# Kernel optimization log

Measured on AMD Instinct MI355X. Metric: run time of the kernel, lower is better.

## Reference

```python
import jax, jax.numpy as jnp
import numpy as np

N = 50000      # nodes
E = 800000     # edges
H = 128        # hidden_channels
L = 3          # num_layers
G = 128        # graphs in batch
MAXZ = 1000    # max_z


def layer_norm(x, g, b, eps=1e-5):
    m = x.mean(-1, keepdims=True)
    v = ((x - m) ** 2).mean(-1, keepdims=True)
    return (x - m) / jnp.sqrt(v + eps) * g + b


def setup_inputs() -> dict:
    key = jax.random.key(0)
    ks = jax.random.split(key, 16)
    z = jax.random.randint(ks[0], (N,), 0, 3)
    edge_index = jax.random.randint(ks[1], (2, E), 0, N)
    batch = jnp.sort(jax.random.randint(ks[2], (N,), 0, G))
    sc = 1.0 / np.sqrt(H)
    z_table = jax.random.normal(ks[3], (MAXZ, H), jnp.float32) * 0.05
    W1s = jax.random.normal(ks[4], (L, H, H), jnp.float32) * sc
    b1s = jnp.zeros((L, H), jnp.float32)
    W2s = jax.random.normal(ks[5], (L, H, H), jnp.float32) * sc
    b2s = jnp.zeros((L, H), jnp.float32)
    lng = jnp.ones((L, H), jnp.float32)
    lnb = jnp.zeros((L, H), jnp.float32)
    lin0_W = jax.random.normal(ks[6], (L * H, H), jnp.float32) * (1.0 / np.sqrt(L * H))
    lin0_b = jnp.zeros((H,), jnp.float32)
    linA_W = jax.random.normal(ks[7], (H, H), jnp.float32) * sc
    linA_b = jnp.zeros((H,), jnp.float32)
    linB_W = jax.random.normal(ks[8], (H, 1), jnp.float32) * sc
    linB_b = jnp.zeros((1,), jnp.float32)
    return dict(z=z, edge_index=edge_index, batch=batch, z_table=z_table,
                W1s=W1s, b1s=b1s, W2s=W2s, b2s=b2s, lng=lng, lnb=lnb,
                lin0_W=lin0_W, lin0_b=lin0_b, linA_W=linA_W, linA_b=linA_b,
                linB_W=linB_W, linB_b=linB_b)


def reference(z, edge_index, batch, z_table, W1s, b1s, W2s, b2s, lng, lnb,
              lin0_W, lin0_b, linA_W, linA_b, linB_W, linB_b):
    # z_emb indices: ([[1],[2]] == z) -> {0,1}, shape [2, N]
    idx = jnp.stack([(z == 1), (z == 2)]).astype(jnp.int32)
    x = z_table[idx]                                  # [2, N, H]
    src, dst = edge_index[0], edge_index[1]
    xs = []
    for l in range(L):
        # GINConv, eps=0: MLP(x + scatter_add of neighbor features)
        agg = jnp.zeros_like(x).at[:, dst].add(x[:, src])   # [2, N, H]
        h = x + agg
        h = jax.nn.relu(h @ W1s[l] + b1s[l])
        h = jax.nn.relu(h @ W2s[l] + b2s[l])
        x = layer_norm(h, lng[l], lnb[l])
        xs.append(x)
    x = jnp.concatenate(xs, axis=-1)                  # [2, N, L*H] (JK)
    # lin0 (dropout = identity in eval), then sum over the label dim
    x = jax.nn.relu(x @ lin0_W + lin0_b).sum(axis=0)  # [N, H]
    # global mean pool over graphs
    sums = jax.ops.segment_sum(x, batch, num_segments=G)                       # [G, H]
    cnt = jax.ops.segment_sum(jnp.ones((x.shape[0], 1), x.dtype), batch, num_segments=G)
    x = sums / jnp.maximum(cnt, 1.0)
    x = jax.nn.relu(x @ linA_W + linA_b)
    return x @ linB_W + linB_b                        # [G, 1]
```

## Files before the change

### kernel.cpp

```cpp
#include <hip/hip_runtime.h>
#include <math.h>

#define NN 50000
#define EE 800000
#define HH 128
#define LL 3
#define GG 128
#define MM (2*NN)
#define PB1 1024

typedef unsigned int u32;
typedef unsigned short u16;
using s16x8 = __attribute__((ext_vector_type(8))) short;
using f32x4 = __attribute__((ext_vector_type(4))) float;

__device__ __forceinline__ u16 f2bf(float f){
  u32 u = __float_as_uint(f);
  return (u16)((u + 0x7fffu + ((u >> 16) & 1u)) >> 16);
}
__device__ __forceinline__ float bf2f(u16 h){ return __uint_as_float(((u32)h) << 16); }
__device__ __forceinline__ u32 splitpack(float v){
  u16 h = f2bf(v);
  float r = v - bf2f(h);
  u16 l = f2bf(r);
  return (u32)h | ((u32)l << 16);
}
__device__ __forceinline__ float unpack2(u32 u){
  return __uint_as_float(u << 16) + __uint_as_float(u & 0xffff0000u);
}

__global__ void zero_i32(int* p, int n){
  int i = blockIdx.x*blockDim.x + threadIdx.x;
  if (i < n) p[i] = 0;
}

__global__ void deg_kernel(const int* __restrict__ ei, int* __restrict__ deg){
  int e = blockIdx.x*blockDim.x + threadIdx.x;
  if (e < EE) atomicAdd(&deg[ei[EE + e]], 1);
}

__global__ void scan_kernel(const int* deg, int* rowstart, int* cursor, int n){
  __shared__ int wsum[16], woff[16];
  __shared__ int carry_s;
  const int tid = threadIdx.x, lane = tid & 63, wid = tid >> 6;
  if (tid == 0) carry_s = 0;
  __syncthreads();
  for (int base = 0; base < n; base += 4096){
    int i4 = base + tid*4;
    int4 v = make_int4(0,0,0,0);
    if (i4 + 3 < n) v = *(const int4*)&deg[i4];
    else {
      if (i4+0 < n) v.x = deg[i4+0];
      if (i4+1 < n) v.y = deg[i4+1];
      if (i4+2 < n) v.z = deg[i4+2];
      if (i4+3 < n) v.w = deg[i4+3];
    }
    int s = v.x + v.y + v.z + v.w;
    int incl = s;
    #pragma unroll
    for (int off = 1; off < 64; off <<= 1){
      int t = __shfl_up(incl, off);
      if (lane >= off) incl += t;
    }
    if (lane == 63) wsum[wid] = incl;
    __syncthreads();
    if (tid < 16){
      int wv = wsum[tid];
      int winc = wv;
      #pragma unroll
      for (int off = 1; off < 16; off <<= 1){
        int t = __shfl_up(winc, off);
        if (tid >= off) winc += t;
      }
      woff[tid] = winc - wv;
    }
    __syncthreads();
    int c = carry_s;
    int excl = c + woff[wid] + incl - s;
    if (i4 < n){
      int p = excl;
      rowstart[i4] = p; cursor[i4] = p; p += v.x;
      if (i4+1 < n){ rowstart[i4+1] = p; cursor[i4+1] = p; p += v.y; }
      if (i4+2 < n){ rowstart[i4+2] = p; cursor[i4+2] = p; p += v.z; }
      if (i4+3 < n){ rowstart[i4+3] = p; cursor[i4+3] = p; }
    }
    __syncthreads();
    if (tid == 1023) carry_s = c + woff[15] + incl;
    __syncthreads();
  }
  if (tid == 0) rowstart[n] = carry_s;
}

__global__ void scatter_kernel(const int* __restrict__ ei, int* __restrict__ cursor,
                               int* __restrict__ csr){
  int e = blockIdx.x*blockDim.x + threadIdx.x;
  if (e < EE){
    int d = ei[EE + e];
    int w = atomicAdd(&cursor[d], 1);
    csr[w] = ei[e];
  }
}

__global__ void prep_w(const float* __restrict__ W1s, const float* __restrict__ W2s,
                       const float* __restrict__ lin0W, u16* __restrict__ wt){
  int idx = blockIdx.x*256 + threadIdx.x;
  int srcsel = idx / 49152;
  int r = idx - srcsel*49152;
  int k = r >> 7, c = r & 127;
  const float* src = srcsel==0 ? W1s : (srcsel==1 ? W2s : lin0W);
  float v = src[r];
  u16 h = f2bf(v);
  u16 l = f2bf(v - bf2f(h));
  if (srcsel < 2){
    int ly = k >> 7, kk = k & 127;
    size_t o = (size_t)srcsel*98304 + (size_t)ly*32768 + (size_t)c*128 + kk;
    wt[o] = h; wt[o + 16384] = l;
  } else {
    size_t o = 196608 + (size_t)c*384 + k;
    wt[o] = h; wt[o + 49152] = l;
  }
}

template<bool L0>
__global__ void agg_kernel(const int* __restrict__ rowstart, const int* __restrict__ csr,
                           const int* __restrict__ z, const float* __restrict__ ztab,
                           const u16* __restrict__ xin,
                           u32* __restrict__ hout){
  const int lane = threadIdx.x & 63;
  const int n    = blockIdx.x*4 + (threadIdx.x >> 6);
  const int e0 = rowstart[n], e1 = rowstart[n+1];
  if (L0){
    const int f2 = lane*2;
    float2 t0 = *(const float2*)&ztab[f2];
    float2 t1 = *(const float2*)&ztab[HH + f2];
    int c1 = 0, c2 = 0;
    for (int base = e0; base < e1; base += 64){
      if (base + lane < e1){
        int zs = z[csr[base + lane]];
        c1 += (zs == 1); c2 += (zs == 2);
      }
    }
    #pragma unroll
    for (int off = 1; off < 64; off <<= 1){
      c1 += __shfl_xor(c1, off);
      c2 += __shfl_xor(c2, off);
    }
    int zn  = z[n];
    int deg = e1 - e0;
    float w1a = (float)((zn == 1) + c1), w0a = (float)((zn != 1) + deg - c1);
    float w1b = (float)((zn == 2) + c2), w0b = (float)((zn != 2) + deg - c2);
    float2 acc0, acc1;
    acc0.x = w1a*t1.x + w0a*t0.x;  acc0.y = w1a*t1.y + w0a*t0.y;
    acc1.x = w1b*t1.x + w0b*t0.x;  acc1.y = w1b*t1.y + w0b*t0.y;
    *(uint2*)(hout + (size_t)n*HH + f2) =
        make_uint2(splitpack(acc0.x), splitpack(acc0.y));
    *(uint2*)(hout + (size_t)(NN + n)*HH + f2) =
        make_uint2(splitpack(acc1.x), splitpack(acc1.y));
  } else {
    const u16* base = xin + lane*4;
    ushort4 sv = *(const ushort4*)(base + (size_t)n*256);
    float4 acc;
    acc.x = bf2f(sv.x); acc.y = bf2f(sv.y);
    acc.z = bf2f(sv.z); acc.w = bf2f(sv.w);
    for (int b = e0; b < e1; b += 64){
      int m  = (e1 - b < 64) ? (e1 - b) : 64;
      int sl = (b + lane < e1) ? csr[b + lane] : 0;
      #pragma unroll 4
      for (int j = 0; j < m; ++j){
        int s = __shfl(sl, j);
        ushort4 v = *(const ushort4*)(base + (size_t)s*256);
        acc.x += bf2f(v.x); acc.y += bf2f(v.y);
        acc.z += bf2f(v.z); acc.w += bf2f(v.w);
      }
    }
    uint4 o;
    o.x = splitpack(acc.x); o.y = splitpack(acc.y);
    o.z = splitpack(acc.z); o.w = splitpack(acc.w);
    const int ch = lane >> 5, f = (lane & 31)*4;
    *(uint4*)(hout + ((size_t)ch*NN + n)*HH + f) = o;
  }
}

template<int K, int MODE>
__global__ __launch_bounds__(256, 4)
void gemm_mfma(const void* __restrict__ Asp,
               const u16* __restrict__ WtHi, const u16* __restrict__ WtLo,
               const float* __restrict__ bias,
               const float* __restrict__ gamma, const float* __restrict__ beta,
               u16* __restrict__ C16, float* __restrict__ Cf){
  constexpr bool ASPLIT = (MODE == 0);
  __shared__ u16 lds[16384];
  const int tid  = threadIdx.x;
  const int lane = tid & 63, w = tid >> 6;
  const int r16  = lane & 15, g = lane >> 4;
  const int rowBase = blockIdx.x * 128;

  f32x4 acc[2][8];
  #pragma unroll
  for (int i = 0; i < 2; i++)
    #pragma unroll
    for (int j = 0; j < 8; j++) acc[i][j] = (f32x4){0.f,0.f,0.f,0.f};

  const int sr = tid & 127;
  const int kq = tid >> 7;
  const int arow = rowBase + sr;
  const bool avalid = arow < MM;
  const int ach = arow >= NN ? 1 : 0;
  const int an  = arow - ach*NN;

  const u16* whi = WtHi + (size_t)sr*K + kq*16;
  const u16* wlo = WtLo + (size_t)sr*K + kq*16;

  for (int kc = 0; kc < K; kc += 32){
    const int k0 = kc + kq*16;
    if (ASPLIT){
      const u32* ap = (const u32*)Asp + (size_t)arow*128 + k0;
      #pragma unroll
      for (int q = 0; q < 4; q++){
        uint4 av = make_uint4(0,0,0,0);
        if (avalid) av = *(const uint4*)(ap + q*4);
        u32 h01 = (av.x & 0xffffu) | (av.y << 16);
        u32 h23 = (av.z & 0xffffu) | (av.w << 16);
        u32 l01 = (av.x >> 16) | (av.y & 0xffff0000u);
        u32 l23 = (av.z >> 16) | (av.w & 0xffff0000u);
        int k = kq*16 + q*4;
        int base = ((k >> 3)*128 + sr)*8 + (k & 7);
        *(uint2*)&lds[base]        = make_uint2(h01, h23);
        *(uint2*)&lds[4096 + base] = make_uint2(l01, l23);
      }
    } else {
      const u16* ap;
      if (MODE == 2)
        ap = (const u16*)Asp + ((size_t)(k0 >> 7))*NN*256 + (size_t)an*256 + ach*128 + (k0 & 127);
      else
        ap = (const u16*)Asp + (size_t)arow*128 + k0;
      #pragma unroll
      for (int hg = 0; hg < 2; hg++){
        uint4 av = make_uint4(0,0,0,0);
        if (avalid) av = *(const uint4*)(ap + hg*8);
        *(uint4*)&lds[((kq*2 + hg)*128 + sr)*8] = av;
      }
    }
    #pragma unroll
    for (int hg = 0; hg < 2; hg++){
      int gsel = kq*2 + hg;
      *(uint4*)&lds[8192  + (gsel*128 + sr)*8] = *(const uint4*)(whi + kc + hg*8);
      *(uint4*)&lds[12288 + (gsel*128 + sr)*8] = *(const uint4*)(wlo + kc + hg*8);
    }
    __syncthreads();
    s16x8 ahi[2], alo[2];
    #pragma unroll
    for (int i = 0; i < 2; i++){
      int idx = (g*128 + w*32 + i*16 + r16)*8;
      ahi[i] = *(const s16x8*)&lds[idx];
      if (ASPLIT) alo[i] = *(const s16x8*)&lds[4096 + idx];
    }
    #pragma unroll
    for (int j = 0; j < 8; j++){
      int bidx = (g*128 + j*16 + r16)*8;
      s16x8 bhi = *(const s16x8*)&lds[8192  + bidx];
      s16x8 blo = *(const s16x8*)&lds[12288 + bidx];
      #pragma unroll
      for (int i = 0; i < 2; i++){
        acc[i][j] = __builtin_amdgcn_mfma_f32_16x16x32_bf16(ahi[i], bhi, acc[i][j], 0, 0, 0);
        acc[i][j] = __builtin_amdgcn_mfma_f32_16x16x32_bf16(ahi[i], blo, acc[i][j], 0, 0, 0);
        if (ASPLIT)
          acc[i][j] = __builtin_amdgcn_mfma_f32_16x16x32_bf16(alo[i], bhi, acc[i][j], 0, 0, 0);
      }
    }
    __syncthreads();
  }

  float bb[8];
  #pragma unroll
  for (int j = 0; j < 8; j++) bb[j] = bias[j*16 + r16];
  #pragma unroll
  for (int i = 0; i < 2; i++)
    #pragma unroll
    for (int j = 0; j < 8; j++)
      #pragma unroll
      for (int c = 0; c < 4; c++){
        float t = acc[i][j][c] + bb[j];
        acc[i][j][c] = t > 0.f ? t : 0.f;
      }

  if (MODE == 1){
    float gg_[8], be[8];
    #pragma unroll
    for (int j = 0; j < 8; j++){ gg_[j] = gamma[j*16 + r16]; be[j] = beta[j*16 + r16]; }
    float mn[2][4], rs[2][4];
    #pragma unroll
    for (int i = 0; i < 2; i++)
      #pragma unroll
      for (int c = 0; c < 4; c++){
        float ss = 0.f, qq = 0.f;
        #pragma unroll
        for (int j = 0; j < 8; j++){ float t = acc[i][j][c]; ss += t; qq += t*t; }
        #pragma unroll
        for (int off = 1; off < 16; off <<= 1){
          ss += __shfl_xor(ss, off);
          qq += __shfl_xor(qq, off);
        }
        float m   = ss * (1.f/128.f);
        float var = qq * (1.f/128.f) - m*m;
        mn[i][c] = m;
        rs[i][c] = rsqrtf(var + 1e-5f);
      }
    #pragma unroll
    for (int i = 0; i < 2; i++)
      #pragma unroll
      for (int j = 0; j < 8; j++)
        #pragma unroll
        for (int c = 0; c < 4; c++)
          acc[i][j][c] = (acc[i][j][c] - mn[i][c]) * rs[i][c] * gg_[j] + be[j];
  }

  #pragma unroll
  for (int i = 0; i < 2; i++)
    #pragma unroll
    for (int c = 0; c < 4; c++){
      int grow = rowBase + w*32 + i*16 + g*4 + c;
      if (grow < MM){
        int cch = grow >= NN ? 1 : 0;
        int cn  = grow - cch*NN;
        #pragma unroll
        for (int j = 0; j < 8; j++){
          int col = j*16 + r16;
          if (MODE == 0)      C16[(size_t)grow*128 + col] = f2bf(acc[i][j][c]);
          else if (MODE == 1) C16[(size_t)cn*256 + cch*128 + col] = f2bf(acc[i][j][c]);
          else                Cf [(size_t)grow*128 + col] = acc[i][j][c];
        }
      }
    }
}

__global__ void pool1_kernel(const float* __restrict__ y2, const int* __restrict__ batch,
                             float* __restrict__ sums){
  const int npb = (NN + PB1 - 1)/PB1;
  int n0 = blockIdx.x * npb;
  if (n0 >= NN) return;
  int n1 = n0 + npb; if (n1 > NN) n1 = NN;
  const int f = threadIdx.x;
  float acc = 0.f;
  int g = batch[n0];
  for (int n = n0; n < n1; n++){
    int bg = batch[n];
    if (bg != g){
      atomicAdd(&sums[(size_t)g*HH + f], acc);
      acc = 0.f; g = bg;
    }
    acc += y2[(size_t)n*HH + f] + y2[(size_t)(NN + n)*HH + f];
  }
  atomicAdd(&sums[(size_t)g*HH + f], acc);
}

__global__ void pool2_kernel(const float* __restrict__ sums, const int* __restrict__ batch,
                             const float* __restrict__ WA, const float* __restrict__ bA,
                             const float* __restrict__ WB, const float* __restrict__ bB,
                             float* __restrict__ out){
  const int g = blockIdx.x, tid = threadIdx.x;
  __shared__ int se[2];
  if (tid < 2){
    int target = g + tid;
    int lo = 0, hi = NN;
    while (lo < hi){ int mid = (lo + hi) >> 1; if (batch[mid] < target) lo = mid + 1; else hi = mid; }
    se[tid] = lo;
  }
  __syncthreads();
  float cnt = (float)(se[1] - se[0]); if (cnt < 1.f) cnt = 1.f;
  __shared__ float ms[HH];
  ms[tid] = sums[(size_t)g*HH + tid] / cnt;
  __syncthreads();
  float t = bA[tid];
  #pragma unroll 8
  for (int k = 0; k < HH; k++) t = fmaf(ms[k], WA[k*HH + tid], t);
  t = t > 0.f ? t : 0.f;
  float v = t * WB[tid];
  #pragma unroll
  for (int off = 32; off >= 1; off >>= 1) v += __shfl_down(v, off);
  __shared__ float r2[2];
  if ((tid & 63) == 0) r2[tid >> 6] = v;
  __syncthreads();
  if (tid == 0) out[g] = r2[0] + r2[1] + bB[0];
}

extern "C" void kernel_launch(void* const* d_in, const int* in_sizes, int n_in,
                              void* d_out, int out_size, void* d_ws, size_t ws_size,
                              hipStream_t stream){
  const int*   z     = (const int*)  d_in[0];
  const int*   ei    = (const int*)  d_in[1];
  const int*   batch = (const int*)  d_in[2];
  const float* ztab  = (const float*)d_in[3];
  const float* W1s   = (const float*)d_in[4];
  const float* b1s   = (const float*)d_in[5];
  const float* W2s   = (const float*)d_in[6];
  const float* b2s   = (const float*)d_in[7];
  const float* lng   = (const float*)d_in[8];
  const float* lnb   = (const float*)d_in[9];
  const float* lin0W = (const float*)d_in[10];
  const float* lin0b = (const float*)d_in[11];
  const float* linAW = (const float*)d_in[12];
  const float* linAb = (const float*)d_in[13];
  const float* linBW = (const float*)d_in[14];
  const float* linBb = (const float*)d_in[15];
  float* out = (float*)d_out;

  char* ws = (char*)d_ws;
  size_t off = 0;
  auto alloc = [&](size_t bytes)->char*{
    char* p = ws + off;
    off = (off + bytes + 255) & ~(size_t)255;
    return p;
  };
  u16* xc       = (u16*)alloc((size_t)LL*NN*256*2);
  u32* h_sp     = (u32*)alloc((size_t)MM*HH*4);
  float* y      = (float*)h_sp;
  u16* t16      = (u16*)alloc((size_t)MM*HH*2);
  u16* wt       = (u16*)alloc(294912*2);
  float* sums   = (float*)alloc((size_t)GG*HH*4);
  int* rowstart = (int*)alloc((size_t)(NN+1)*4);
  int* cursor   = (int*)alloc((size_t)NN*4);
  int* csr      = (int*)alloc((size_t)EE*4);

  const int gemmGrid = (MM + 127)/128;

  prep_w<<<576, 256, 0, stream>>>(W1s, W2s, lin0W, wt);

  zero_i32<<<(NN + 255)/256, 256, 0, stream>>>(cursor, NN);
  zero_i32<<<(GG*HH)/256, 256, 0, stream>>>((int*)sums, GG*HH);
  deg_kernel<<<EE/256, 256, 0, stream>>>(ei, cursor);
  scan_kernel<<<1, 1024, 0, stream>>>(cursor, rowstart, cursor, NN);
  scatter_kernel<<<EE/256, 256, 0, stream>>>(ei, cursor, csr);

  for (int l = 0; l < LL; l++){
    if (l == 0)
      agg_kernel<true ><<<NN/4, 256, 0, stream>>>(rowstart, csr, z, ztab, nullptr, h_sp);
    else
      agg_kernel<false><<<NN/4, 256, 0, stream>>>(rowstart, csr, z, ztab,
                                                  xc + (size_t)(l-1)*NN*256, h_sp);
    gemm_mfma<128,0><<<gemmGrid, 256, 0, stream>>>(
        h_sp, wt + l*32768, wt + l*32768 + 16384,
        b1s + l*HH, nullptr, nullptr, t16, nullptr);
    gemm_mfma<128,1><<<gemmGrid, 256, 0, stream>>>(
        t16, wt + 98304 + l*32768, wt + 98304 + l*32768 + 16384,
        b2s + l*HH, lng + l*HH, lnb + l*HH, xc + (size_t)l*NN*256, nullptr);
  }
  gemm_mfma<384,2><<<gemmGrid, 256, 0, stream>>>(
      xc, wt + 196608, wt + 245760,
      lin0b, nullptr, nullptr, nullptr, y);
  pool1_kernel<<<PB1, HH, 0, stream>>>(y, batch, sums);
  pool2_kernel<<<GG, HH, 0, stream>>>(sums, batch, linAW, linAb, linBW, linBb, out);
}
```

Baseline: 591.5 us.

## Fuse the two GIN MLP GEMMs per layer and store lin0 output as bf16

Merges the first and second MLP GEMMs of each GIN layer into one kernel. The intermediate activation stays in LDS as bf16 instead of going through a global buffer, which removes a write and a read of a 2N x 128 tensor per layer. The lin0 GEMM becomes its own kernel that writes bf16 output instead of fp32, and the pooling kernel reads bf16, halving that traffic. In exchange, LDS use per block rises and occupancy drops to 3 blocks per CU, and the lin0 output is rounded to bf16 before pooling.

```diff
diff --git a/kernel.cpp b/kernel.cpp
--- a/kernel.cpp
+++ b/kernel.cpp
@@ -24,9 +24,6 @@
   float r = v - bf2f(h);
   u16 l = f2bf(r);
   return (u32)h | ((u32)l << 16);
-}
-__device__ __forceinline__ float unpack2(u32 u){
-  return __uint_as_float(u << 16) + __uint_as_float(u & 0xffff0000u);
 }
 
 __global__ void zero_i32(int* p, int n){
@@ -181,71 +178,55 @@
   }
 }
 
-template<int K, int MODE>
-__global__ __launch_bounds__(256, 4)
-void gemm_mfma(const void* __restrict__ Asp,
-               const u16* __restrict__ WtHi, const u16* __restrict__ WtLo,
-               const float* __restrict__ bias,
+__global__ __launch_bounds__(256, 3)
+void mlp_fused(const u32* __restrict__ hsp,
+               const u16* __restrict__ W1hi, const u16* __restrict__ W1lo,
+               const float* __restrict__ b1,
+               const u16* __restrict__ W2hi, const u16* __restrict__ W2lo,
+               const float* __restrict__ b2,
                const float* __restrict__ gamma, const float* __restrict__ beta,
-               u16* __restrict__ C16, float* __restrict__ Cf){
-  constexpr bool ASPLIT = (MODE == 0);
-  __shared__ u16 lds[16384];
+               u16* __restrict__ xcout){
+  __shared__ u16 lds[24576];
   const int tid  = threadIdx.x;
   const int lane = tid & 63, w = tid >> 6;
   const int r16  = lane & 15, g = lane >> 4;
   const int rowBase = blockIdx.x * 128;
 
-  f32x4 acc[2][8];
-  #pragma unroll
-  for (int i = 0; i < 2; i++)
-    #pragma unroll
-    for (int j = 0; j < 8; j++) acc[i][j] = (f32x4){0.f,0.f,0.f,0.f};
-
   const int sr = tid & 127;
   const int kq = tid >> 7;
   const int arow = rowBase + sr;
   const bool avalid = arow < MM;
-  const int ach = arow >= NN ? 1 : 0;
-  const int an  = arow - ach*NN;
-
-  const u16* whi = WtHi + (size_t)sr*K + kq*16;
-  const u16* wlo = WtLo + (size_t)sr*K + kq*16;
-
-  for (int kc = 0; kc < K; kc += 32){
+
+  f32x4 acc[2][8];
+  #pragma unroll
+  for (int i = 0; i < 2; i++)
+    #pragma unroll
+    for (int j = 0; j < 8; j++) acc[i][j] = (f32x4){0.f,0.f,0.f,0.f};
+
+  const u16* whi1 = W1hi + (size_t)sr*128 + kq*16;
+  const u16* wlo1 = W1lo + (size_t)sr*128 + kq*16;
+
+  for (int kc = 0; kc < 128; kc += 32){
     const int k0 = kc + kq*16;
-    if (ASPLIT){
-      const u32* ap = (const u32*)Asp + (size_t)arow*128 + k0;
-      #pragma unroll
-      for (int q = 0; q < 4; q++){
-        uint4 av = make_uint4(0,0,0,0);
-        if (avalid) av = *(const uint4*)(ap + q*4);
-        u32 h01 = (av.x & 0xffffu) | (av.y << 16);
-        u32 h23 = (av.z & 0xffffu) | (av.w << 16);
-        u32 l01 = (av.x >> 16) | (av.y & 0xffff0000u);
-        u32 l23 = (av.z >> 16) | (av.w & 0xffff0000u);
-        int k = kq*16 + q*4;
-        int base = ((k >> 3)*128 + sr)*8 + (k & 7);
-        *(uint2*)&lds[base]        = make_uint2(h01, h23);
-        *(uint2*)&lds[4096 + base] = make_uint2(l01, l23);
-      }
-    } else {
-      const u16* ap;
-      if (MODE == 2)
-        ap = (const u16*)Asp + ((size_t)(k0 >> 7))*NN*256 + (size_t)an*256 + ach*128 + (k0 & 127);
-      else
-        ap = (const u16*)Asp + (size_t)arow*128 + k0;
-      #pragma unroll
-      for (int hg = 0; hg < 2; hg++){
-        uint4 av = make_uint4(0,0,0,0);
-        if (avalid) av = *(const uint4*)(ap + hg*8);
-        *(uint4*)&lds[((kq*2 + hg)*128 + sr)*8] = av;
-      }
+    const u32* ap = hsp + (size_t)arow*128 + k0;
+    #pragma unroll
+    for (int q = 0; q < 4; q++){
+      uint4 av = make_uint4(0,0,0,0);
+      if (avalid) av = *(const uint4*)(ap + q*4);
+      u32 h01 = (av.x & 0xffffu) | (av.y << 16);
+      u32 h23 = (av.z & 0xffffu) | (av.w << 16);
+      u32 l01 = (av.x >> 16) | (av.y & 0xffff0000u);
+      u32 l23 = (av.z >> 16) | (av.w & 0xffff0000u);
+      int k = kq*16 + q*4;
+      int base = ((k >> 3)*128 + sr)*8 + (k & 7);
+      *(uint2*)&lds[base]        = make_uint2(h01, h23);
+      *(uint2*)&lds[4096 + base] = make_uint2(l01, l23);
     }
     #pragma unroll
     for (int hg = 0; hg < 2; hg++){
       int gsel = kq*2 + hg;
-      *(uint4*)&lds[8192  + (gsel*128 + sr)*8] = *(const uint4*)(whi + kc + hg*8);
-      *(uint4*)&lds[12288 + (gsel*128 + sr)*8] = *(const uint4*)(wlo + kc + hg*8);
+      *(uint4*)&lds[8192  + (gsel*128 + sr)*8] = *(const uint4*)(whi1 + kc + hg*8);
+      *(uint4*)&lds[12288 + (gsel*128 + sr)*8] = *(const uint4*)(wlo1 + kc + hg*8);
     }
     __syncthreads();
     s16x8 ahi[2], alo[2];
@@ -253,7 +234,7 @@
     for (int i = 0; i < 2; i++){
       int idx = (g*128 + w*32 + i*16 + r16)*8;
       ahi[i] = *(const s16x8*)&lds[idx];
-      if (ASPLIT) alo[i] = *(const s16x8*)&lds[4096 + idx];
+      alo[i] = *(const s16x8*)&lds[4096 + idx];
     }
     #pragma unroll
     for (int j = 0; j < 8; j++){
@@ -264,57 +245,103 @@
       for (int i = 0; i < 2; i++){
         acc[i][j] = __builtin_amdgcn_mfma_f32_16x16x32_bf16(ahi[i], bhi, acc[i][j], 0, 0, 0);
         acc[i][j] = __builtin_amdgcn_mfma_f32_16x16x32_bf16(ahi[i], blo, acc[i][j], 0, 0, 0);
-        if (ASPLIT)
-          acc[i][j] = __builtin_amdgcn_mfma_f32_16x16x32_bf16(alo[i], bhi, acc[i][j], 0, 0, 0);
-      }
-    }
-    __syncthreads();
-  }
-
-  float bb[8];
-  #pragma unroll
-  for (int j = 0; j < 8; j++) bb[j] = bias[j*16 + r16];
+        acc[i][j] = __builtin_amdgcn_mfma_f32_16x16x32_bf16(alo[i], bhi, acc[i][j], 0, 0, 0);
+      }
+    }
+    __syncthreads();
+  }
+
+  {
+    float bb[8];
+    #pragma unroll
+    for (int j = 0; j < 8; j++) bb[j] = b1[j*16 + r16];
+    #pragma unroll
+    for (int i = 0; i < 2; i++)
+      #pragma unroll
+      for (int c = 0; c < 4; c++){
+        int row = w*32 + i*16 + g*4 + c;
+        #pragma unroll
+        for (int j = 0; j < 8; j++){
+          int col = j*16 + r16;
+          float t = acc[i][j][c] + bb[j];
+          t = t > 0.f ? t : 0.f;
+          lds[((col >> 3)*128 + row)*8 + (col & 7)] = f2bf(t);
+        }
+      }
+  }
+  __syncthreads();
+
+  f32x4 acc2[2][8];
+  #pragma unroll
+  for (int i = 0; i < 2; i++)
+    #pragma unroll
+    for (int j = 0; j < 8; j++) acc2[i][j] = (f32x4){0.f,0.f,0.f,0.f};
+
+  const u16* whi2 = W2hi + (size_t)sr*128 + kq*16;
+  const u16* wlo2 = W2lo + (size_t)sr*128 + kq*16;
+
+  for (int kc = 0; kc < 128; kc += 32){
+    #pragma unroll
+    for (int hg = 0; hg < 2; hg++){
+      int gsel = kq*2 + hg;
+      *(uint4*)&lds[16384 + (gsel*128 + sr)*8] = *(const uint4*)(whi2 + kc + hg*8);
+      *(uint4*)&lds[20480 + (gsel*128 + sr)*8] = *(const uint4*)(wlo2 + kc + hg*8);
+    }
+    __syncthreads();
+    s16x8 a2[2];
+    #pragma unroll
+    for (int i = 0; i < 2; i++){
+      int oct = (kc >> 3) + g;
+      a2[i] = *(const s16x8*)&lds[(oct*128 + w*32 + i*16 + r16)*8];
+    }
+    #pragma unroll
+    for (int j = 0; j < 8; j++){
+      int bidx = (g*128 + j*16 + r16)*8;
+      s16x8 bhi = *(const s16x8*)&lds[16384 + bidx];
+      s16x8 blo = *(const s16x8*)&lds[20480 + bidx];
+      #pragma unroll
+      for (int i = 0; i < 2; i++){
+        acc2[i][j] = __builtin_amdgcn_mfma_f32_16x16x32_bf16(a2[i], bhi, acc2[i][j], 0, 0, 0);
+        acc2[i][j] = __builtin_amdgcn_mfma_f32_16x16x32_bf16(a2[i], blo, acc2[i][j], 0, 0, 0);
+      }
+    }
+    __syncthreads();
+  }
+
+  float bb[8], gg_[8], be[8];
+  #pragma unroll
+  for (int j = 0; j < 8; j++){
+    bb[j]  = b2[j*16 + r16];
+    gg_[j] = gamma[j*16 + r16];
+    be[j]  = beta[j*16 + r16];
+  }
   #pragma unroll
   for (int i = 0; i < 2; i++)
     #pragma unroll
     for (int j = 0; j < 8; j++)
       #pragma unroll
       for (int c = 0; c < 4; c++){
-        float t = acc[i][j][c] + bb[j];
-        acc[i][j][c] = t > 0.f ? t : 0.f;
-      }
-
-  if (MODE == 1){
-    float gg_[8], be[8];
-    #pragma unroll
-    for (int j = 0; j < 8; j++){ gg_[j] = gamma[j*16 + r16]; be[j] = beta[j*16 + r16]; }
-    float mn[2][4], rs[2][4];
-    #pragma unroll
-    for (int i = 0; i < 2; i++)
-      #pragma unroll
-      for (int c = 0; c < 4; c++){
-        float ss = 0.f, qq = 0.f;
-        #pragma unroll
-        for (int j = 0; j < 8; j++){ float t = acc[i][j][c]; ss += t; qq += t*t; }
-        #pragma unroll
-        for (int off = 1; off < 16; off <<= 1){
-          ss += __shfl_xor(ss, off);
-          qq += __shfl_xor(qq, off);
-        }
-        float m   = ss * (1.f/128.f);
-        float var = qq * (1.f/128.f) - m*m;
-        mn[i][c] = m;
-        rs[i][c] = rsqrtf(var + 1e-5f);
-      }
-    #pragma unroll
-    for (int i = 0; i < 2; i++)
-      #pragma unroll
-      for (int j = 0; j < 8; j++)
-        #pragma unroll
-        for (int c = 0; c < 4; c++)
-          acc[i][j][c] = (acc[i][j][c] - mn[i][c]) * rs[i][c] * gg_[j] + be[j];
-  }
-
+        float t = acc2[i][j][c] + bb[j];
+        acc2[i][j][c] = t > 0.f ? t : 0.f;
+      }
+  float mn[2][4], rs[2][4];
+  #pragma unroll
+  for (int i = 0; i < 2; i++)
+    #pragma unroll
+    for (int c = 0; c < 4; c++){
+      float ss = 0.f, qq = 0.f;
+      #pragma unroll
+      for (int j = 0; j < 8; j++){ float t = acc2[i][j][c]; ss += t; qq += t*t; }
+      #pragma unroll
+      for (int off = 1; off < 16; off <<= 1){
+        ss += __shfl_xor(ss, off);
+        qq += __shfl_xor(qq, off);
+      }
+      float m   = ss * (1.f/128.f);
+      float var = qq * (1.f/128.f) - m*m;
+      mn[i][c] = m;
+      rs[i][c] = rsqrtf(var + 1e-5f);
+    }
   #pragma unroll
   for (int i = 0; i < 2; i++)
     #pragma unroll
@@ -326,15 +353,93 @@
         #pragma unroll
         for (int j = 0; j < 8; j++){
           int col = j*16 + r16;
-          if (MODE == 0)      C16[(size_t)grow*128 + col] = f2bf(acc[i][j][c]);
-          else if (MODE == 1) C16[(size_t)cn*256 + cch*128 + col] = f2bf(acc[i][j][c]);
-          else                Cf [(size_t)grow*128 + col] = acc[i][j][c];
+          float v = (acc2[i][j][c] - mn[i][c]) * rs[i][c] * gg_[j] + be[j];
+          xcout[(size_t)cn*256 + cch*128 + col] = f2bf(v);
         }
       }
     }
 }
 
-__global__ void pool1_kernel(const float* __restrict__ y2, const int* __restrict__ batch,
+__global__ __launch_bounds__(256, 4)
+void gemm_lin0(const u16* __restrict__ Axc,
+               const u16* __restrict__ WtHi, const u16* __restrict__ WtLo,
+               const float* __restrict__ bias, u16* __restrict__ Y16){
+  __shared__ u16 lds[16384];
+  const int tid  = threadIdx.x;
+  const int lane = tid & 63, w = tid >> 6;
+  const int r16  = lane & 15, g = lane >> 4;
+  const int rowBase = blockIdx.x * 128;
+
+  f32x4 acc[2][8];
+  #pragma unroll
+  for (int i = 0; i < 2; i++)
+    #pragma unroll
+    for (int j = 0; j < 8; j++) acc[i][j] = (f32x4){0.f,0.f,0.f,0.f};
+
+  const int sr = tid & 127;
+  const int kq = tid >> 7;
+  const int arow = rowBase + sr;
+  const bool avalid = arow < MM;
+  const int ach = arow >= NN ? 1 : 0;
+  const int an  = arow - ach*NN;
+
+  const u16* whi = WtHi + (size_t)sr*384 + kq*16;
+  const u16* wlo = WtLo + (size_t)sr*384 + kq*16;
+
+  for (int kc = 0; kc < 384; kc += 32){
+    const int k0 = kc + kq*16;
+    const u16* ap = Axc + ((size_t)(k0 >> 7))*NN*256 + (size_t)an*256 + ach*128 + (k0 & 127);
+    #pragma unroll
+    for (int hg = 0; hg < 2; hg++){
+      uint4 av = make_uint4(0,0,0,0);
+      if (avalid) av = *(const uint4*)(ap + hg*8);
+      *(uint4*)&lds[((kq*2 + hg)*128 + sr)*8] = av;
+    }
+    #pragma unroll
+    for (int hg = 0; hg < 2; hg++){
+      int gsel = kq*2 + hg;
+      *(uint4*)&lds[8192  + (gsel*128 + sr)*8] = *(const uint4*)(whi + kc + hg*8);
+      *(uint4*)&lds[12288 + (gsel*128 + sr)*8] = *(const uint4*)(wlo + kc + hg*8);
+    }
+    __syncthreads();
+    s16x8 ahi[2];
+    #pragma unroll
+    for (int i = 0; i < 2; i++)
+      ahi[i] = *(const s16x8*)&lds[(g*128 + w*32 + i*16 + r16)*8];
+    #pragma unroll
+    for (int j = 0; j < 8; j++){
+      int bidx = (g*128 + j*16 + r16)*8;
+      s16x8 bhi = *(const s16x8*)&lds[8192  + bidx];
+      s16x8 blo = *(const s16x8*)&lds[12288 + bidx];
+      #pragma unroll
+      for (int i = 0; i < 2; i++){
+        acc[i][j] = __builtin_amdgcn_mfma_f32_16x16x32_bf16(ahi[i], bhi, acc[i][j], 0, 0, 0);
+        acc[i][j] = __builtin_amdgcn_mfma_f32_16x16x32_bf16(ahi[i], blo, acc[i][j], 0, 0, 0);
+      }
+    }
+    __syncthreads();
+  }
+
+  float bb[8];
+  #pragma unroll
+  for (int j = 0; j < 8; j++) bb[j] = bias[j*16 + r16];
+  #pragma unroll
+  for (int i = 0; i < 2; i++)
+    #pragma unroll
+    for (int c = 0; c < 4; c++){
+      int grow = rowBase + w*32 + i*16 + g*4 + c;
+      if (grow < MM){
+        #pragma unroll
+        for (int j = 0; j < 8; j++){
+          float t = acc[i][j][c] + bb[j];
+          t = t > 0.f ? t : 0.f;
+          Y16[(size_t)grow*128 + j*16 + r16] = f2bf(t);
+        }
+      }
+    }
+}
+
+__global__ void pool1_kernel(const u16* __restrict__ y16, const int* __restrict__ batch,
                              float* __restrict__ sums){
   const int npb = (NN + PB1 - 1)/PB1;
   int n0 = blockIdx.x * npb;
@@ -349,7 +454,7 @@
       atomicAdd(&sums[(size_t)g*HH + f], acc);
       acc = 0.f; g = bg;
     }
-    acc += y2[(size_t)n*HH + f] + y2[(size_t)(NN + n)*HH + f];
+    acc += bf2f(y16[(size_t)n*HH + f]) + bf2f(y16[(size_t)(NN + n)*HH + f]);
   }
   atomicAdd(&sums[(size_t)g*HH + f], acc);
 }
@@ -414,8 +519,7 @@
   };
   u16* xc       = (u16*)alloc((size_t)LL*NN*256*2);
   u32* h_sp     = (u32*)alloc((size_t)MM*HH*4);
-  float* y      = (float*)h_sp;
-  u16* t16      = (u16*)alloc((size_t)MM*HH*2);
+  u16* y16      = (u16*)h_sp;
   u16* wt       = (u16*)alloc(294912*2);
   float* sums   = (float*)alloc((size_t)GG*HH*4);
   int* rowstart = (int*)alloc((size_t)(NN+1)*4);
@@ -438,16 +542,14 @@
     else
       agg_kernel<false><<<NN/4, 256, 0, stream>>>(rowstart, csr, z, ztab,
                                                   xc + (size_t)(l-1)*NN*256, h_sp);
-    gemm_mfma<128,0><<<gemmGrid, 256, 0, stream>>>(
-        h_sp, wt + l*32768, wt + l*32768 + 16384,
-        b1s + l*HH, nullptr, nullptr, t16, nullptr);
-    gemm_mfma<128,1><<<gemmGrid, 256, 0, stream>>>(
-        t16, wt + 98304 + l*32768, wt + 98304 + l*32768 + 16384,
-        b2s + l*HH, lng + l*HH, lnb + l*HH, xc + (size_t)l*NN*256, nullptr);
-  }
-  gemm_mfma<384,2><<<gemmGrid, 256, 0, stream>>>(
-      xc, wt + 196608, wt + 245760,
-      lin0b, nullptr, nullptr, nullptr, y);
-  pool1_kernel<<<PB1, HH, 0, stream>>>(y, batch, sums);
+    mlp_fused<<<gemmGrid, 256, 0, stream>>>(
+        h_sp,
+        wt + l*32768, wt + l*32768 + 16384, b1s + l*HH,
+        wt + 98304 + l*32768, wt + 98304 + l*32768 + 16384, b2s + l*HH,
+        lng + l*HH, lnb + l*HH,
+        xc + (size_t)l*NN*256);
+  }
+  gemm_lin0<<<gemmGrid, 256, 0, stream>>>(xc, wt + 196608, wt + 245760, lin0b, y16);
+  pool1_kernel<<<PB1, HH, 0, stream>>>(y16, batch, sums);
   pool2_kernel<<<GG, HH, 0, stream>>>(sums, batch, linAW, linAb, linBW, linBb, out);
 }
```

Measured after the change: 561.2 us. 1.05x faster.
